# Kernel optimization log

Hardware: AMD Instinct MI355X
Metric: run time of the kernel (lower is better)

The kernel has to match this reference:

```python
import jax, jax.numpy as jnp
import numpy as np

EMBED_DIM = 1024
NUM_HEADS = 16
HEAD_DIM = EMBED_DIM // NUM_HEADS


def setup_inputs() -> dict:
    key = jax.random.key(0)
    kx, kq, kk, kv, ko = jax.random.split(key, 5)
    scale = 1.0 / np.sqrt(EMBED_DIM)
    return {
        "x": jax.random.normal(kx, (4, 2048, EMBED_DIM), dtype=jnp.float32),
        # nn.Linear weights are [out, in]; y = x @ W.T
        "w_q": jax.random.normal(kq, (EMBED_DIM, EMBED_DIM), dtype=jnp.float32) * scale,
        "w_k": jax.random.normal(kk, (EMBED_DIM, EMBED_DIM), dtype=jnp.float32) * scale,
        "w_v": jax.random.normal(kv, (EMBED_DIM, EMBED_DIM), dtype=jnp.float32) * scale,
        "w_o": jax.random.normal(ko, (EMBED_DIM, EMBED_DIM), dtype=jnp.float32) * scale,
    }


def reference(x, w_q, w_k, w_v, w_o):
    b, s, _ = x.shape
    # projections (Linear with no bias: x @ W.T)
    q = (x @ w_q.T).reshape(b, s, NUM_HEADS, HEAD_DIM).transpose(0, 2, 1, 3)
    k = (x @ w_k.T).reshape(b, s, NUM_HEADS, HEAD_DIM).transpose(0, 2, 1, 3)
    v = (x @ w_v.T).reshape(b, s, NUM_HEADS, HEAD_DIM).transpose(0, 2, 1, 3)
    # scores: [b, h, s, s]
    scores = jnp.einsum("bhqd,bhkd->bhqk", q, k) / jnp.sqrt(jnp.float32(HEAD_DIM)).astype(x.dtype)
    attn = jax.nn.softmax(scores, axis=-1)
    out = jnp.einsum("bhqk,bhkd->bhqd", attn, v)  # [b, h, s, d]
    out = out.transpose(0, 2, 1, 3).reshape(b, s, EMBED_DIM)
    return out @ w_o.T
```

## Files before the change

### kernel.cpp

```cpp
#include <hip/hip_runtime.h>
#include <math.h>

#define EMBED 1024
#define NHEAD 16
#define HDIM  64
#define BATCH 4
#define SEQ   2048
#define MROWS (BATCH * SEQ)

typedef __attribute__((ext_vector_type(4))) short short4v;
typedef __attribute__((ext_vector_type(8))) short short8;
typedef __attribute__((ext_vector_type(4))) float floatx4;
typedef __attribute__((ext_vector_type(16))) float floatx16;
typedef __attribute__((ext_vector_type(2))) unsigned uint2v;

#if __has_builtin(__builtin_amdgcn_exp2f)
#define EXP2(x) __builtin_amdgcn_exp2f(x)
#else
#define EXP2(x) exp2f(x)
#endif

__device__ __forceinline__ unsigned short f2bf(float f) {
  unsigned u = __float_as_uint(f);
  u += 0x7fffu + ((u >> 16) & 1u);
  return (unsigned short)(u >> 16);
}

#if __has_builtin(__builtin_amdgcn_cvt_pk_bf16_f32)
__device__ __forceinline__ unsigned pack2bf(float lo, float hi) {
  typedef __attribute__((ext_vector_type(2))) __bf16 bf2;
  union { bf2 b; unsigned u; } c;
  c.b = __builtin_amdgcn_cvt_pk_bf16_f32(lo, hi);
  return c.u;
}
#else
__device__ __forceinline__ unsigned pack2bf(float lo, float hi) {
  return ((__float_as_uint(lo) + 0x8000u) >> 16) |
         ((__float_as_uint(hi) + 0x8000u) & 0xffff0000u);
}
#endif

__device__ __forceinline__ uint2v pl32swap(unsigned a, unsigned b) {
#if __has_builtin(__builtin_amdgcn_permlane32_swap)
  return __builtin_amdgcn_permlane32_swap(a, b, false, false);
#else
  uint2v r;
  unsigned ax = (unsigned)__shfl_xor((int)a, 32);
  unsigned bx = (unsigned)__shfl_xor((int)b, 32);
  const int hi = (int)((threadIdx.x & 63) >> 5);
  r[0] = hi ? bx : a;
  r[1] = hi ? b : ax;
  return r;
#endif
}

__device__ __forceinline__ void gl_lds16(const void* g, void* l) {
  __builtin_amdgcn_global_load_lds(
      (const __attribute__((address_space(1))) unsigned int*)g,
      (__attribute__((address_space(3))) unsigned int*)l, 16, 0, 0);
}

__global__ __launch_bounds__(256) void cast_bf16_kernel(
    const float* __restrict__ x,  const float* __restrict__ wq,
    const float* __restrict__ wk, const float* __restrict__ wv,
    const float* __restrict__ wo,
    unsigned short* __restrict__ xb, unsigned short* __restrict__ wb) {
  const size_t NX = (size_t)MROWS * EMBED;
  size_t i4 = ((size_t)blockIdx.x * 256 + threadIdx.x) * 4;
  const float* src;
  unsigned short* dst;
  size_t off;
  if (i4 < NX) {
    src = x; dst = xb; off = i4;
  } else {
    size_t j = i4 - NX;
    int r = (int)(j >> 20);
    off = j & ((1u << 20) - 1);
    src = (r == 0) ? wq : (r == 1) ? wk : (r == 2) ? wv : wo;
    dst = wb + ((size_t)r << 20);
  }
  float4 v = *(const float4*)(src + off);
  ushort4 o;
  o.x = f2bf(v.x); o.y = f2bf(v.y); o.z = f2bf(v.z); o.w = f2bf(v.w);
  *(ushort4*)(dst + off) = o;
}

__device__ __forceinline__ void gemm_core(
    const unsigned short* __restrict__ Amat,
    const unsigned short* __restrict__ Bmat,
    int mBase, int nBase,
    unsigned short* As, unsigned short* Bs,
    floatx4 acc[4][4]) {
  const int t = threadIdx.x;
  const int lane = t & 63, w = t >> 6;
  const int wr = w >> 1, wc = w & 1;
  const int quad = lane >> 4, l15 = lane & 15;

  const int f0 = (w * 2 + 0) * 64 + lane;
  const int f1 = (w * 2 + 1) * 64 + lane;
  const unsigned short* ga0 = Amat + (size_t)(mBase + (f0 >> 2)) * EMBED + (f0 & 3) * 8;
  const unsigned short* ga1 = Amat + (size_t)(mBase + (f1 >> 2)) * EMBED + (f1 & 3) * 8;
  const unsigned short* gb0 = Bmat + (size_t)(nBase + (f0 >> 2)) * EMBED + (f0 & 3) * 8;
  const unsigned short* gb1 = Bmat + (size_t)(nBase + (f1 >> 2)) * EMBED + (f1 & 3) * 8;
  unsigned short* la0 = As + (w * 2 + 0) * 512;
  unsigned short* la1 = As + (w * 2 + 1) * 512;
  unsigned short* lb0 = Bs + (w * 2 + 0) * 512;
  unsigned short* lb1 = Bs + (w * 2 + 1) * 512;

  for (int kb = 0; kb < EMBED; kb += 32) {
    __syncthreads();
    gl_lds16(ga0 + kb, la0);
    gl_lds16(ga1 + kb, la1);
    gl_lds16(gb0 + kb, lb0);
    gl_lds16(gb1 + kb, lb1);
    __syncthreads();
    short8 a[4], b[4];
#pragma unroll
    for (int mi = 0; mi < 4; ++mi)
      a[mi] = *(const short8*)&As[(wr * 64 + mi * 16 + l15) * 32 + quad * 8];
#pragma unroll
    for (int ni = 0; ni < 4; ++ni)
      b[ni] = *(const short8*)&Bs[(wc * 64 + ni * 16 + l15) * 32 + quad * 8];
#pragma unroll
    for (int mi = 0; mi < 4; ++mi)
#pragma unroll
      for (int ni = 0; ni < 4; ++ni)
        acc[mi][ni] = __builtin_amdgcn_mfma_f32_16x16x32_bf16(
            a[mi], b[ni], acc[mi][ni], 0, 0, 0);
  }
}

__global__ __launch_bounds__(256) void proj_qkv_bf16(
    const unsigned short* __restrict__ xb,
    const unsigned short* __restrict__ wb,
    unsigned short* __restrict__ qkv) {
  const int id = blockIdx.x;
  const int xcd = id & 7;
  const int r = id >> 3;
  const int which = r >> 6;
  const int rm = r & 63;
  const int mBase = (xcd * 8 + (rm >> 3)) * 128;
  const int nBase = (rm & 7) * 128;

  const unsigned short* W = wb + ((size_t)which << 20);

  __shared__ unsigned short As[128 * 32];
  __shared__ unsigned short Bs[128 * 32];

  floatx4 acc[4][4] = {};
  gemm_core(xb, W, mBase, nBase, As, Bs, acc);

  const int t = threadIdx.x;
  const int lane = t & 63, w = t >> 6;
  const int wr = w >> 1, wc = w & 1;
  const int quad = lane >> 4, l15 = lane & 15;

  unsigned short* out = qkv + (size_t)which * MROWS * EMBED;
  if (which < 2) {
    const float scale = (which == 0) ? 0.18033688f : 1.0f;
#pragma unroll
    for (int mi = 0; mi < 4; ++mi)
#pragma unroll
      for (int ni = 0; ni < 4; ++ni) {
        const int n = nBase + wc * 64 + ni * 16 + l15;
        const int h = n >> 6, d = n & 63;
#pragma unroll
        for (int r2 = 0; r2 < 4; ++r2) {
          const int m = mBase + wr * 64 + mi * 16 + quad * 4 + r2;
          const int b = m >> 11, s = m & (SEQ - 1);
          out[(((size_t)(b * NHEAD + h) * SEQ) + s) * HDIM + d] =
              f2bf(acc[mi][ni][r2] * scale);
        }
      }
  } else {
#pragma unroll
    for (int mi = 0; mi < 4; ++mi) {
      const int m0 = mBase + wr * 64 + mi * 16 + quad * 4;
      const int b = m0 >> 11, s0 = m0 & (SEQ - 1);
#pragma unroll
      for (int ni = 0; ni < 4; ++ni) {
        const int n = nBase + wc * 64 + ni * 16 + l15;
        const int h = n >> 6, d = n & 63;
        ushort4 pk;
        pk.x = f2bf(acc[mi][ni][0]); pk.y = f2bf(acc[mi][ni][1]);
        pk.z = f2bf(acc[mi][ni][2]); pk.w = f2bf(acc[mi][ni][3]);
        *(ushort4*)&out[((size_t)(b * NHEAD + h) * HDIM + d) * SEQ + s0] = pk;
      }
    }
  }
}

__global__ __launch_bounds__(256, 2) void attn_mfma(
    const unsigned short* __restrict__ qkv,
    unsigned short* __restrict__ aout) {
  const unsigned short* Q = qkv;
  const unsigned short* K = qkv + (size_t)MROWS * EMBED;
  const unsigned short* V = qkv + 2 * (size_t)MROWS * EMBED;

  const int id = blockIdx.x;
  const int xcd = id & 7, slot = id >> 3;
  const int bh = xcd * 8 + (slot >> 3);
  const int qBase = (slot & 7) * 256;

  __shared__ unsigned short Ks[2 * 128 * 64];
  __shared__ unsigned short Vs[2 * 64 * 128];

  const int t = threadIdx.x;
  const int lane = t & 63, w = t >> 6;
  const int h2 = lane >> 5;
  const int q31 = lane & 31;

  const unsigned short* qrowA =
      Q + ((size_t)bh * SEQ + qBase + w * 64 + q31) * HDIM;
  const unsigned short* qrowB = qrowA + 32 * HDIM;
  short8 qaA[4], qaB[4];
#pragma unroll
  for (int ds = 0; ds < 4; ++ds) {
    qaA[ds] = *(const short8*)(qrowA + ds * 16 + h2 * 8);
    qaB[ds] = *(const short8*)(qrowB + ds * 16 + h2 * 8);
  }

  const unsigned short* kbase = K + (size_t)bh * SEQ * HDIM;
  const unsigned short* vbase = V + (size_t)bh * HDIM * SEQ;
  const unsigned short* gk[4];
  const unsigned short* gv[4];
  unsigned short* lk[4];
  unsigned short* lv[4];
#pragma unroll
  for (int i = 0; i < 4; ++i) {
    const int c = i * 256 + t;
    const int krow = c >> 3, kgrp = (c & 7) ^ (krow & 7);
    gk[i] = kbase + (size_t)krow * HDIM + kgrp * 8;
    const int vd = c >> 4, vj = (c & 15) ^ (vd & 15);
    gv[i] = vbase + (size_t)vd * SEQ + vj * 8;
    const int cu = i * 256 + w * 64;
    lk[i] = Ks + cu * 8;
    lv[i] = Vs + cu * 8;
  }

  floatx16 otA0 = {}, otA1 = {};
  floatx16 otB0 = {}, otB1 = {};
  float laccA = 0.0f, laccB = 0.0f;

#pragma unroll
  for (int i = 0; i < 4; ++i) {
    gl_lds16(gk[i], lk[i]);
    gl_lds16(gv[i], lv[i]);
  }

  for (int kt = 0; kt < SEQ; kt += 128) {
    const int cb = (kt >> 7) & 1;
    const int nb = cb ^ 1;
    const int nxt = (kt + 128) & (SEQ - 1);
    const int sOff = nb * 8192;
#pragma unroll
    for (int i = 0; i < 4; ++i) {
      gl_lds16(gk[i] + (size_t)nxt * HDIM, lk[i] + sOff);
      gl_lds16(gv[i] + nxt, lv[i] + sOff);
    }
    __builtin_amdgcn_sched_barrier(0);
    asm volatile("s_waitcnt vmcnt(8)" ::: "memory");
    __builtin_amdgcn_s_barrier();

    const int kOff = cb * 8192;
    const int vOff = cb * 8192;

#pragma unroll
    for (int sub = 0; sub < 2; ++sub) {
      const int koff = sub * 64;
#pragma unroll
      for (int kh = 0; kh < 2; ++kh) {
        const int krow = koff + kh * 32 + q31;
        floatx16 stA = {}, stB = {};
        __builtin_amdgcn_s_setprio(1);
#pragma unroll
        for (int ds = 0; ds < 4; ++ds) {
          const int g = ds * 2 + h2;
          short8 ka = *(const short8*)&Ks[kOff + krow * 64 + ((g ^ (q31 & 7)) * 8)];
          stA = __builtin_amdgcn_mfma_f32_32x32x16_bf16(ka, qaA[ds], stA, 0, 0, 0);
          stB = __builtin_amdgcn_mfma_f32_32x32x16_bf16(ka, qaB[ds], stB, 0, 0, 0);
        }
        __builtin_amdgcn_s_setprio(0);

#pragma unroll
        for (int spp = 0; spp < 2; ++spp) {
          unsigned pA[4], pB[4];
#pragma unroll
          for (int i = 0; i < 4; ++i) {
            float a0 = EXP2(stA[8 * spp + 2 * i]);
            float a1 = EXP2(stA[8 * spp + 2 * i + 1]);
            laccA += a0 + a1;
            pA[i] = pack2bf(a0, a1);
            float b0 = EXP2(stB[8 * spp + 2 * i]);
            float b1 = EXP2(stB[8 * spp + 2 * i + 1]);
            laccB += b0 + b1;
            pB[i] = pack2bf(b0, b1);
          }
          uint2v ra0 = pl32swap(pA[0], pA[2]);
          uint2v ra1 = pl32swap(pA[1], pA[3]);
          uint2v rb0 = pl32swap(pB[0], pB[2]);
          uint2v rb1 = pl32swap(pB[1], pB[3]);
          union { unsigned u[4]; short8 v; } pbA, pbB;
          pbA.u[0] = ra0[0]; pbA.u[1] = ra1[0]; pbA.u[2] = ra0[1]; pbA.u[3] = ra1[1];
          pbB.u[0] = rb0[0]; pbB.u[1] = rb1[0]; pbB.u[2] = rb0[1]; pbB.u[3] = rb1[1];

          const int g8 = sub * 8 + (kh * 2 + spp) * 2 + h2;
          const int pos = (g8 ^ (q31 & 15)) * 8;
          short8 va0 = *(const short8*)&Vs[vOff + q31 * 128 + pos];
          short8 va1 = *(const short8*)&Vs[vOff + (32 + q31) * 128 + pos];
          otA0 = __builtin_amdgcn_mfma_f32_32x32x16_bf16(va0, pbA.v, otA0, 0, 0, 0);
          otB0 = __builtin_amdgcn_mfma_f32_32x32x16_bf16(va0, pbB.v, otB0, 0, 0, 0);
          otA1 = __builtin_amdgcn_mfma_f32_32x32x16_bf16(va1, pbA.v, otA1, 0, 0, 0);
          otB1 = __builtin_amdgcn_mfma_f32_32x32x16_bf16(va1, pbB.v, otB1, 0, 0, 0);
        }
      }
    }

    __builtin_amdgcn_sched_barrier(0);
    __builtin_amdgcn_s_barrier();
  }
  asm volatile("s_waitcnt vmcnt(0)" ::: "memory");

  const float totA = laccA + __shfl_xor(laccA, 32);
  const float totB = laccB + __shfl_xor(laccB, 32);
  const float invA = 1.0f / totA;
  const float invB = 1.0f / totB;

  const int b = bh >> 4, hh = bh & 15;
  unsigned short* orowA =
      aout + ((size_t)b * SEQ + qBase + w * 64 + q31) * EMBED + hh * HDIM;
  unsigned short* orowB = orowA + (size_t)32 * EMBED;
#pragma unroll
  for (int rg = 0; rg < 4; ++rg) {
    const int d0 = rg * 8 + h2 * 4;
    ushort4 p0, p1;
    p0.x = f2bf(otA0[4 * rg + 0] * invA); p0.y = f2bf(otA0[4 * rg + 1] * invA);
    p0.z = f2bf(otA0[4 * rg + 2] * invA); p0.w = f2bf(otA0[4 * rg + 3] * invA);
    *(ushort4*)(orowA + d0) = p0;
    p1.x = f2bf(otA1[4 * rg + 0] * invA); p1.y = f2bf(otA1[4 * rg + 1] * invA);
    p1.z = f2bf(otA1[4 * rg + 2] * invA); p1.w = f2bf(otA1[4 * rg + 3] * invA);
    *(ushort4*)(orowA + 32 + d0) = p1;
    ushort4 p2, p3;
    p2.x = f2bf(otB0[4 * rg + 0] * invB); p2.y = f2bf(otB0[4 * rg + 1] * invB);
    p2.z = f2bf(otB0[4 * rg + 2] * invB); p2.w = f2bf(otB0[4 * rg + 3] * invB);
    *(ushort4*)(orowB + d0) = p2;
    p3.x = f2bf(otB1[4 * rg + 0] * invB); p3.y = f2bf(otB1[4 * rg + 1] * invB);
    p3.z = f2bf(otB1[4 * rg + 2] * invB); p3.w = f2bf(otB1[4 * rg + 3] * invB);
    *(ushort4*)(orowB + 32 + d0) = p3;
  }
}

__global__ __launch_bounds__(256) void out_proj_bf16(
    const unsigned short* __restrict__ aout,
    const unsigned short* __restrict__ wb,
    float* __restrict__ Cout) {
  const int id = blockIdx.x;
  const int xcd = id & 7;
  const int r = id >> 3;
  const int mBase = (xcd * 8 + (r >> 3)) * 128;
  const int nBase = (r & 7) * 128;

  __shared__ unsigned short As[128 * 32];
  __shared__ unsigned short Bs[128 * 32];

  floatx4 acc[4][4] = {};
  gemm_core(aout, wb + ((size_t)3 << 20), mBase, nBase, As, Bs, acc);

  const int t = threadIdx.x;
  const int lane = t & 63, w = t >> 6;
  const int wr = w >> 1, wc = w & 1;
  const int quad = lane >> 4, l15 = lane & 15;

#pragma unroll
  for (int mi = 0; mi < 4; ++mi)
#pragma unroll
    for (int ni = 0; ni < 4; ++ni) {
      const int n = nBase + wc * 64 + ni * 16 + l15;
#pragma unroll
      for (int r2 = 0; r2 < 4; ++r2) {
        const int m = mBase + wr * 64 + mi * 16 + quad * 4 + r2;
        Cout[(size_t)m * EMBED + n] = acc[mi][ni][r2];
      }
    }
}

extern "C" void kernel_launch(void* const* d_in, const int* in_sizes, int n_in,
                              void* d_out, int out_size, void* d_ws, size_t ws_size,
                              hipStream_t stream) {
  const float* x  = (const float*)d_in[0];
  const float* wq = (const float*)d_in[1];
  const float* wk = (const float*)d_in[2];
  const float* wv = (const float*)d_in[3];
  const float* wo = (const float*)d_in[4];
  float* out = (float*)d_out;

  char* ws = (char*)d_ws;
  unsigned short* xb   = (unsigned short*)(ws);
  unsigned short* wb   = (unsigned short*)(ws + (16u << 20));
  unsigned short* qkv  = (unsigned short*)(ws + (26u << 20));
  unsigned short* aout = (unsigned short*)(ws + (76u << 20));

  cast_bf16_kernel<<<12288, 256, 0, stream>>>(x, wq, wk, wv, wo, xb, wb);
  proj_qkv_bf16<<<1536, 256, 0, stream>>>(xb, wb, qkv);
  attn_mfma<<<512, 256, 0, stream>>>(qkv, aout);
  out_proj_bf16<<<512, 256, 0, stream>>>(aout, wb, out);
}
```

Measured before the change: 270.0 us.

## Split attention key range across warp pairs and reduce partial outputs in LDS

```diff
diff --git a/kernel.cpp b/kernel.cpp
--- a/kernel.cpp
+++ b/kernel.cpp
@@ -190,7 +190,7 @@
   }
 }
 
-__global__ __launch_bounds__(256, 2) void attn_mfma(
+__global__ __launch_bounds__(256, 4) void attn_mfma(
     const unsigned short* __restrict__ qkv,
     unsigned short* __restrict__ aout) {
   const unsigned short* Q = qkv;
@@ -199,19 +199,21 @@
 
   const int id = blockIdx.x;
   const int xcd = id & 7, slot = id >> 3;
-  const int bh = xcd * 8 + (slot >> 3);
-  const int qBase = (slot & 7) * 256;
-
-  __shared__ unsigned short Ks[2 * 128 * 64];
-  __shared__ unsigned short Vs[2 * 64 * 128];
+  const int bh = xcd * 8 + (slot >> 4);
+  const int qBase = (slot & 15) * 128;
+
+  __shared__ unsigned short SM[16384];
+  __shared__ float lsum[2][64][2];
 
   const int t = threadIdx.x;
   const int lane = t & 63, w = t >> 6;
+  const int qh = w & 1;
+  const int kh = w >> 1;
   const int h2 = lane >> 5;
   const int q31 = lane & 31;
 
   const unsigned short* qrowA =
-      Q + ((size_t)bh * SEQ + qBase + w * 64 + q31) * HDIM;
+      Q + ((size_t)bh * SEQ + qBase + qh * 64 + q31) * HDIM;
   const unsigned short* qrowB = qrowA + 32 * HDIM;
   short8 qaA[4], qaB[4];
 #pragma unroll
@@ -222,20 +224,19 @@
 
   const unsigned short* kbase = K + (size_t)bh * SEQ * HDIM;
   const unsigned short* vbase = V + (size_t)bh * HDIM * SEQ;
-  const unsigned short* gk[4];
-  const unsigned short* gv[4];
-  unsigned short* lk[4];
-  unsigned short* lv[4];
-#pragma unroll
-  for (int i = 0; i < 4; ++i) {
-    const int c = i * 256 + t;
-    const int krow = c >> 3, kgrp = (c & 7) ^ (krow & 7);
-    gk[i] = kbase + (size_t)krow * HDIM + kgrp * 8;
-    const int vd = c >> 4, vj = (c & 15) ^ (vd & 15);
-    gv[i] = vbase + (size_t)vd * SEQ + vj * 8;
+  const unsigned short* gk[2];
+  const unsigned short* gv[2];
+  unsigned short* lk[2];
+  unsigned short* lv[2];
+#pragma unroll
+  for (int i = 0; i < 2; ++i) {
+    const int krow = t >> 3, kgrp = (t & 7) ^ (krow & 7);
+    gk[i] = kbase + ((size_t)(i * 1024 + krow)) * HDIM + kgrp * 8;
+    const int vd = t >> 2, vj = (t & 3) ^ (vd & 3);
+    gv[i] = vbase + (size_t)vd * SEQ + i * 1024 + vj * 8;
     const int cu = i * 256 + w * 64;
-    lk[i] = Ks + cu * 8;
-    lv[i] = Vs + cu * 8;
+    lk[i] = SM + cu * 8;
+    lv[i] = SM + 8192 + cu * 8;
   }
 
   floatx16 otA0 = {}, otA1 = {};
@@ -243,110 +244,132 @@
   float laccA = 0.0f, laccB = 0.0f;
 
 #pragma unroll
-  for (int i = 0; i < 4; ++i) {
+  for (int i = 0; i < 2; ++i) {
     gl_lds16(gk[i], lk[i]);
     gl_lds16(gv[i], lv[i]);
   }
 
-  for (int kt = 0; kt < SEQ; kt += 128) {
-    const int cb = (kt >> 7) & 1;
+  for (int kt = 0; kt < 1024; kt += 32) {
+    const int cb = (kt >> 5) & 1;
     const int nb = cb ^ 1;
-    const int nxt = (kt + 128) & (SEQ - 1);
-    const int sOff = nb * 8192;
-#pragma unroll
-    for (int i = 0; i < 4; ++i) {
+    const int nxt = (kt + 32) & 1023;
+    const int sOff = nb * 4096;
+#pragma unroll
+    for (int i = 0; i < 2; ++i) {
       gl_lds16(gk[i] + (size_t)nxt * HDIM, lk[i] + sOff);
       gl_lds16(gv[i] + nxt, lv[i] + sOff);
     }
     __builtin_amdgcn_sched_barrier(0);
-    asm volatile("s_waitcnt vmcnt(8)" ::: "memory");
+    asm volatile("s_waitcnt vmcnt(4)" ::: "memory");
     __builtin_amdgcn_s_barrier();
 
-    const int kOff = cb * 8192;
-    const int vOff = cb * 8192;
-
-#pragma unroll
-    for (int sub = 0; sub < 2; ++sub) {
-      const int koff = sub * 64;
-#pragma unroll
-      for (int kh = 0; kh < 2; ++kh) {
-        const int krow = koff + kh * 32 + q31;
-        floatx16 stA = {}, stB = {};
-        __builtin_amdgcn_s_setprio(1);
-#pragma unroll
-        for (int ds = 0; ds < 4; ++ds) {
-          const int g = ds * 2 + h2;
-          short8 ka = *(const short8*)&Ks[kOff + krow * 64 + ((g ^ (q31 & 7)) * 8)];
-          stA = __builtin_amdgcn_mfma_f32_32x32x16_bf16(ka, qaA[ds], stA, 0, 0, 0);
-          stB = __builtin_amdgcn_mfma_f32_32x32x16_bf16(ka, qaB[ds], stB, 0, 0, 0);
-        }
-        __builtin_amdgcn_s_setprio(0);
-
-#pragma unroll
-        for (int spp = 0; spp < 2; ++spp) {
-          unsigned pA[4], pB[4];
-#pragma unroll
-          for (int i = 0; i < 4; ++i) {
-            float a0 = EXP2(stA[8 * spp + 2 * i]);
-            float a1 = EXP2(stA[8 * spp + 2 * i + 1]);
-            laccA += a0 + a1;
-            pA[i] = pack2bf(a0, a1);
-            float b0 = EXP2(stB[8 * spp + 2 * i]);
-            float b1 = EXP2(stB[8 * spp + 2 * i + 1]);
-            laccB += b0 + b1;
-            pB[i] = pack2bf(b0, b1);
-          }
-          uint2v ra0 = pl32swap(pA[0], pA[2]);
-          uint2v ra1 = pl32swap(pA[1], pA[3]);
-          uint2v rb0 = pl32swap(pB[0], pB[2]);
-          uint2v rb1 = pl32swap(pB[1], pB[3]);
-          union { unsigned u[4]; short8 v; } pbA, pbB;
-          pbA.u[0] = ra0[0]; pbA.u[1] = ra1[0]; pbA.u[2] = ra0[1]; pbA.u[3] = ra1[1];
-          pbB.u[0] = rb0[0]; pbB.u[1] = rb1[0]; pbB.u[2] = rb0[1]; pbB.u[3] = rb1[1];
-
-          const int g8 = sub * 8 + (kh * 2 + spp) * 2 + h2;
-          const int pos = (g8 ^ (q31 & 15)) * 8;
-          short8 va0 = *(const short8*)&Vs[vOff + q31 * 128 + pos];
-          short8 va1 = *(const short8*)&Vs[vOff + (32 + q31) * 128 + pos];
-          otA0 = __builtin_amdgcn_mfma_f32_32x32x16_bf16(va0, pbA.v, otA0, 0, 0, 0);
-          otB0 = __builtin_amdgcn_mfma_f32_32x32x16_bf16(va0, pbB.v, otB0, 0, 0, 0);
-          otA1 = __builtin_amdgcn_mfma_f32_32x32x16_bf16(va1, pbA.v, otA1, 0, 0, 0);
-          otB1 = __builtin_amdgcn_mfma_f32_32x32x16_bf16(va1, pbB.v, otB1, 0, 0, 0);
-        }
-      }
-    }
+    const int kOff = cb * 4096 + kh * 2048;
+    const int vOff = 8192 + cb * 4096 + kh * 2048;
+
+    floatx16 stA = {}, stB = {};
+    __builtin_amdgcn_s_setprio(1);
+#pragma unroll
+    for (int ds = 0; ds < 4; ++ds) {
+      const int g = ds * 2 + h2;
+      short8 ka = *(const short8*)&SM[kOff + q31 * 64 + ((g ^ (q31 & 7)) * 8)];
+      stA = __builtin_amdgcn_mfma_f32_32x32x16_bf16(ka, qaA[ds], stA, 0, 0, 0);
+      stB = __builtin_amdgcn_mfma_f32_32x32x16_bf16(ka, qaB[ds], stB, 0, 0, 0);
+    }
+    __builtin_amdgcn_s_setprio(0);
+
+    unsigned pA[8], pB[8];
+#pragma unroll
+    for (int i = 0; i < 8; ++i) {
+      float a0 = EXP2(stA[2 * i]), a1 = EXP2(stA[2 * i + 1]);
+      laccA += a0 + a1;
+      pA[i] = pack2bf(a0, a1);
+      float b0 = EXP2(stB[2 * i]), b1 = EXP2(stB[2 * i + 1]);
+      laccB += b0 + b1;
+      pB[i] = pack2bf(b0, b1);
+    }
+
+    __builtin_amdgcn_s_setprio(1);
+#pragma unroll
+    for (int sp = 0; sp < 2; ++sp) {
+      const int off = sp * 4;
+      uint2v ra0 = pl32swap(pA[off + 0], pA[off + 2]);
+      uint2v ra1 = pl32swap(pA[off + 1], pA[off + 3]);
+      uint2v rb0 = pl32swap(pB[off + 0], pB[off + 2]);
+      uint2v rb1 = pl32swap(pB[off + 1], pB[off + 3]);
+      union { unsigned u[4]; short8 v; } pbA, pbB;
+      pbA.u[0] = ra0[0]; pbA.u[1] = ra1[0]; pbA.u[2] = ra0[1]; pbA.u[3] = ra1[1];
+      pbB.u[0] = rb0[0]; pbB.u[1] = rb1[0]; pbB.u[2] = rb0[1]; pbB.u[3] = rb1[1];
+
+      const int g8 = sp * 2 + h2;
+      const int pos = (g8 ^ (q31 & 3)) * 8;
+      short8 va0 = *(const short8*)&SM[vOff + q31 * 32 + pos];
+      short8 va1 = *(const short8*)&SM[vOff + (32 + q31) * 32 + pos];
+      otA0 = __builtin_amdgcn_mfma_f32_32x32x16_bf16(va0, pbA.v, otA0, 0, 0, 0);
+      otB0 = __builtin_amdgcn_mfma_f32_32x32x16_bf16(va0, pbB.v, otB0, 0, 0, 0);
+      otA1 = __builtin_amdgcn_mfma_f32_32x32x16_bf16(va1, pbA.v, otA1, 0, 0, 0);
+      otB1 = __builtin_amdgcn_mfma_f32_32x32x16_bf16(va1, pbB.v, otB1, 0, 0, 0);
+    }
+    __builtin_amdgcn_s_setprio(0);
 
     __builtin_amdgcn_sched_barrier(0);
     __builtin_amdgcn_s_barrier();
   }
   asm volatile("s_waitcnt vmcnt(0)" ::: "memory");
-
-  const float totA = laccA + __shfl_xor(laccA, 32);
-  const float totB = laccB + __shfl_xor(laccB, 32);
-  const float invA = 1.0f / totA;
-  const float invB = 1.0f / totB;
-
-  const int b = bh >> 4, hh = bh & 15;
-  unsigned short* orowA =
-      aout + ((size_t)b * SEQ + qBase + w * 64 + q31) * EMBED + hh * HDIM;
-  unsigned short* orowB = orowA + (size_t)32 * EMBED;
-#pragma unroll
-  for (int rg = 0; rg < 4; ++rg) {
-    const int d0 = rg * 8 + h2 * 4;
-    ushort4 p0, p1;
-    p0.x = f2bf(otA0[4 * rg + 0] * invA); p0.y = f2bf(otA0[4 * rg + 1] * invA);
-    p0.z = f2bf(otA0[4 * rg + 2] * invA); p0.w = f2bf(otA0[4 * rg + 3] * invA);
-    *(ushort4*)(orowA + d0) = p0;
-    p1.x = f2bf(otA1[4 * rg + 0] * invA); p1.y = f2bf(otA1[4 * rg + 1] * invA);
-    p1.z = f2bf(otA1[4 * rg + 2] * invA); p1.w = f2bf(otA1[4 * rg + 3] * invA);
-    *(ushort4*)(orowA + 32 + d0) = p1;
-    ushort4 p2, p3;
-    p2.x = f2bf(otB0[4 * rg + 0] * invB); p2.y = f2bf(otB0[4 * rg + 1] * invB);
-    p2.z = f2bf(otB0[4 * rg + 2] * invB); p2.w = f2bf(otB0[4 * rg + 3] * invB);
-    *(ushort4*)(orowB + d0) = p2;
-    p3.x = f2bf(otB1[4 * rg + 0] * invB); p3.y = f2bf(otB1[4 * rg + 1] * invB);
-    p3.z = f2bf(otB1[4 * rg + 2] * invB); p3.w = f2bf(otB1[4 * rg + 3] * invB);
-    *(ushort4*)(orowB + 32 + d0) = p3;
+  __syncthreads();
+
+  float* lbuf = (float*)SM;
+  if (kh == 1) {
+    float* dst = lbuf + qh * 4096 + lane;
+#pragma unroll
+    for (int r = 0; r < 16; ++r) {
+      dst[(r) * 64]      = otA0[r];
+      dst[(16 + r) * 64] = otA1[r];
+      dst[(32 + r) * 64] = otB0[r];
+      dst[(48 + r) * 64] = otB1[r];
+    }
+    lsum[qh][lane][0] = laccA;
+    lsum[qh][lane][1] = laccB;
+  }
+  __syncthreads();
+  if (kh == 0) {
+    const float* src = lbuf + qh * 4096 + lane;
+#pragma unroll
+    for (int r = 0; r < 16; ++r) {
+      otA0[r] += src[(r) * 64];
+      otA1[r] += src[(16 + r) * 64];
+      otB0[r] += src[(32 + r) * 64];
+      otB1[r] += src[(48 + r) * 64];
+    }
+    laccA += lsum[qh][lane][0];
+    laccB += lsum[qh][lane][1];
+
+    const float totA = laccA + __shfl_xor(laccA, 32);
+    const float totB = laccB + __shfl_xor(laccB, 32);
+    const float invA = 1.0f / totA;
+    const float invB = 1.0f / totB;
+
+    const int b = bh >> 4, hh = bh & 15;
+    unsigned short* orowA =
+        aout + ((size_t)b * SEQ + qBase + qh * 64 + q31) * EMBED + hh * HDIM;
+    unsigned short* orowB = orowA + (size_t)32 * EMBED;
+#pragma unroll
+    for (int rg = 0; rg < 4; ++rg) {
+      const int d0 = rg * 8 + h2 * 4;
+      ushort4 p0, p1;
+      p0.x = f2bf(otA0[4 * rg + 0] * invA); p0.y = f2bf(otA0[4 * rg + 1] * invA);
+      p0.z = f2bf(otA0[4 * rg + 2] * invA); p0.w = f2bf(otA0[4 * rg + 3] * invA);
+      *(ushort4*)(orowA + d0) = p0;
+      p1.x = f2bf(otA1[4 * rg + 0] * invA); p1.y = f2bf(otA1[4 * rg + 1] * invA);
+      p1.z = f2bf(otA1[4 * rg + 2] * invA); p1.w = f2bf(otA1[4 * rg + 3] * invA);
+      *(ushort4*)(orowA + 32 + d0) = p1;
+      ushort4 p2, p3;
+      p2.x = f2bf(otB0[4 * rg + 0] * invB); p2.y = f2bf(otB0[4 * rg + 1] * invB);
+      p2.z = f2bf(otB0[4 * rg + 2] * invB); p2.w = f2bf(otB0[4 * rg + 3] * invB);
+      *(ushort4*)(orowB + d0) = p2;
+      p3.x = f2bf(otB1[4 * rg + 0] * invB); p3.y = f2bf(otB1[4 * rg + 1] * invB);
+      p3.z = f2bf(otB1[4 * rg + 2] * invB); p3.w = f2bf(otB1[4 * rg + 3] * invB);
+      *(ushort4*)(orowB + 32 + d0) = p3;
+    }
   }
 }
 
@@ -402,6 +425,6 @@
 
   cast_bf16_kernel<<<12288, 256, 0, stream>>>(x, wq, wk, wv, wo, xb, wb);
   proj_qkv_bf16<<<1536, 256, 0, stream>>>(xb, wb, qkv);
-  attn_mfma<<<512, 256, 0, stream>>>(qkv, aout);
+  attn_mfma<<<1024, 256, 0, stream>>>(qkv, aout);
   out_proj_bf16<<<512, 256, 0, stream>>>(aout, wb, out);
 }
```

After: 405.8 us. 1.5x slower.
